# Kernel optimization log

Measured on AMD Instinct MI355X. Metric: run time of the kernel, lower is better.

Reference implementation:

```python
import jax, jax.numpy as jnp
import numpy as np

N = 100000      # nodes
E = 1200000     # edges (avg degree ~12)
D_IN = 64
D_OUT = 64


def setup_inputs() -> dict:
    key = jax.random.key(0)
    k1, k2, k3, k4 = jax.random.split(key, 4)
    x = jax.random.normal(k1, (N, D_IN), dtype=jnp.float32)
    # learned params (glorot-ish init)
    W = jax.random.normal(k2, (D_IN, D_OUT), dtype=jnp.float32) / np.sqrt(D_IN).astype(np.float32)
    b = jnp.zeros((D_OUT,), dtype=jnp.float32)
    src = jax.random.randint(k3, (E,), 0, N, dtype=jnp.int32)
    dst = jax.random.randint(k4, (E,), 0, N, dtype=jnp.int32)
    return {"x": x, "W": W, "b": b, "src": src, "dst": dst}


def reference(x, W, b, src, dst):
    # GCN layer: h = relu( D^-1/2 A D^-1/2 (x @ W) + b ), dropout=0 (eval)
    ones = jnp.ones(src.shape[0], dtype=x.dtype)
    deg_out = jax.ops.segment_sum(ones, src, num_segments=N)   # out-degree of source nodes
    deg_in = jax.ops.segment_sum(ones, dst, num_segments=N)    # in-degree of dest nodes
    norm_src = jax.lax.rsqrt(jnp.maximum(deg_out, 1.0))
    norm_dst = jax.lax.rsqrt(jnp.maximum(deg_in, 1.0))

    h = x @ W                                                  # [N, D_OUT] dense transform
    msg = h[src] * norm_src[src][:, None]                      # [E, D_OUT] gathered, pre-normalized messages
    agg = jax.ops.segment_sum(msg, dst, num_segments=N)        # [N, D_OUT] sparse aggregation
    out = agg * norm_dst[:, None] + b
    return jax.nn.relu(out)
```

## Files before the change

kernel.cpp:

```cpp
#include <hip/hip_runtime.h>
#include <hip/hip_bf16.h>

#define N_NODES 100000
#define N_EDGES 1200000
#define DCH 64

#define HB 96
#define CHUNK ((N_EDGES + HB - 1) / HB)
#define HALF_BINS 50000
#define HALF_WORDS 12500

#define BNODES 256
#define KBUK ((N_NODES + BNODES - 1) / BNODES)
#define CAPE 6144

#define OFF_DEG      0
#define OFF_BPART    512000
#define OFF_BLOCKOFF 665600
#define OFF_FLAG     819200
#define OFF_ESORT    819456
#define OFF_HS       10419712

__device__ __forceinline__ float load_f(const void* p, int i, int f32) {
    if (f32) return ((const float*)p)[i];
    return __bfloat162float(((const __hip_bfloat16*)p)[i]);
}

__device__ __forceinline__ unsigned short f2bf_bits(float f) {
    __hip_bfloat16 h = __float2bfloat16(f);
    return __builtin_bit_cast(unsigned short, h);
}

__global__ __launch_bounds__(1024)
void edges_kernel(const int* __restrict__ src,
                  const int* __restrict__ dst,
                  const void* __restrict__ x,
                  unsigned int* __restrict__ deg_packed,
                  int* __restrict__ bpart,
                  int* __restrict__ flag) {
    __shared__ unsigned int h[HALF_WORDS];
    __shared__ int cnt[KBUK];
    int tid = threadIdx.x, b = blockIdx.x, half = blockIdx.y;
    for (int w = tid; w < HALF_WORDS; w += 1024) h[w] = 0;
    if (half == 0)
        for (int i = tid; i < KBUK; i += 1024) cnt[i] = 0;
    __syncthreads();
    int lo = half * HALF_BINS;
    int e0 = b * CHUNK;
    int e1 = e0 + CHUNK; if (e1 > N_EDGES) e1 = N_EDGES;
    for (int e = e0 + tid; e < e1; e += 1024) {
        int n = src[e] - lo;
        if ((unsigned)n < (unsigned)HALF_BINS)
            atomicAdd(&h[n >> 2], 1u << ((n & 3) * 8));
        if (half == 0)
            atomicAdd(&cnt[dst[e] >> 8], 1);
    }
    __syncthreads();
    unsigned int* dp = deg_packed + half * HALF_WORDS;
    for (int w = tid; w < HALF_WORDS; w += 1024) {
        unsigned int v = h[w];
        if (v) atomicAdd(&dp[w], v);
    }
    if (half == 0)
        for (int i = tid; i < KBUK; i += 1024) bpart[b * KBUK + i] = cnt[i];

    if (b == 0 && half == 0) {
        __syncthreads();
        if (tid == 0) cnt[0] = 0;
        __syncthreads();
        if (tid < 256) {
            const unsigned short* u = (const unsigned short*)x;
            int c = 0;
            for (int i = tid * 16; i < tid * 16 + 16; ++i) {
                unsigned short v = u[2 * i];
                int e = (v >> 7) & 0xFF;
                if (e >= 141) c++;
            }
            if (c) atomicAdd(&cnt[0], c);
        }
        __syncthreads();
        if (tid == 0) *flag = (cnt[0] > 256) ? 1 : 0;
    }
}

__global__ void gemm_scale_kernel(const void* __restrict__ x,
                                  const void* __restrict__ W,
                                  const unsigned int* __restrict__ deg_packed,
                                  const int* __restrict__ flag,
                                  __hip_bfloat16* __restrict__ hs) {
    int f32 = *flag;
    int lane = threadIdx.x & 63;
    int wave = (blockIdx.x * blockDim.x + threadIdx.x) >> 6;
    int nwaves = (gridDim.x * blockDim.x) >> 6;

    float wcol[DCH];
#pragma unroll
    for (int k = 0; k < DCH; ++k)
        wcol[k] = load_f(W, k * DCH + lane, f32);

    for (int node = wave; node < N_NODES; node += nwaves) {
        float xv = load_f(x, node * DCH + lane, f32);
        float s0 = 0.0f, s1 = 0.0f, s2 = 0.0f, s3 = 0.0f;
#pragma unroll
        for (int k = 0; k < DCH; k += 4) {
            float x0 = __int_as_float(__builtin_amdgcn_readlane(__float_as_int(xv), k + 0));
            float x1 = __int_as_float(__builtin_amdgcn_readlane(__float_as_int(xv), k + 1));
            float x2 = __int_as_float(__builtin_amdgcn_readlane(__float_as_int(xv), k + 2));
            float x3 = __int_as_float(__builtin_amdgcn_readlane(__float_as_int(xv), k + 3));
            s0 = fmaf(x0, wcol[k + 0], s0);
            s1 = fmaf(x1, wcol[k + 1], s1);
            s2 = fmaf(x2, wcol[k + 2], s2);
            s3 = fmaf(x3, wcol[k + 3], s3);
        }
        float sum = (s0 + s1) + (s2 + s3);
        unsigned int dw = deg_packed[node >> 2];
        float deg = (float)((dw >> ((node & 3) * 8)) & 0xFFu);
        float nrm = rsqrtf(fmaxf(deg, 1.0f));
        hs[node * DCH + lane] = __float2bfloat16(sum * nrm);
    }
}

__global__ __launch_bounds__(512)
void bscan_kernel(const int* __restrict__ bpart, int* __restrict__ blockoff) {
    __shared__ int s[512];
    int k = threadIdx.x;
    int tot = 0;
    if (k < KBUK)
        for (int b = 0; b < HB; ++b) tot += bpart[b * KBUK + k];
    s[k] = tot;
    __syncthreads();
    for (int off = 1; off < 512; off <<= 1) {
        int add = (k >= off) ? s[k - off] : 0;
        __syncthreads();
        s[k] += add;
        __syncthreads();
    }
    if (k < KBUK) {
        int run = s[k] - tot;
        for (int b = 0; b < HB; ++b) {
            blockoff[b * KBUK + k] = run;
            run += bpart[b * KBUK + k];
        }
    }
}

__global__ __launch_bounds__(1024)
void semisort_kernel(const int* __restrict__ src,
                     const int* __restrict__ dst,
                     const int* __restrict__ blockoff,
                     unsigned int* __restrict__ esort) {
    __shared__ int cur[KBUK];
    int tid = threadIdx.x, blk = blockIdx.x;
    for (int i = tid; i < KBUK; i += 1024) cur[i] = blockoff[blk * KBUK + i];
    __syncthreads();
    int e0 = blk * CHUNK;
    int e1 = e0 + CHUNK; if (e1 > N_EDGES) e1 = N_EDGES;
    for (int e = e0 + tid; e < e1; e += 1024) {
        int d = dst[e];
        int pos = atomicAdd(&cur[d >> 8], 1);
        esort[pos] = (unsigned int)src[e] | ((unsigned int)(d & 255) << 24);
    }
}

__global__ __launch_bounds__(1024)
void sortgather_kernel(const __hip_bfloat16* __restrict__ hs,
                       const unsigned int* __restrict__ esort,
                       const int* __restrict__ blockoff,
                       const void* __restrict__ b,
                       const int* __restrict__ flag,
                       void* __restrict__ out) {
    __shared__ unsigned int ebuf[CAPE];
    __shared__ int cnt[BNODES];
    __shared__ int loc[BNODES];
    __shared__ int sc[BNODES];
    __shared__ int cur[BNODES];
    int k = blockIdx.x, tid = threadIdx.x;
    int bbase = blockoff[k];
    int bend  = (k + 1 < KBUK) ? blockoff[k + 1] : N_EDGES;
    int m = bend - bbase;
    if (m > CAPE) m = CAPE;

    if (tid < BNODES) { cnt[tid] = 0; cur[tid] = 0; }
    __syncthreads();
    for (int e = tid; e < m; e += 1024)
        atomicAdd(&cnt[esort[bbase + e] >> 24], 1);
    __syncthreads();
    int v = 0;
    if (tid < BNODES) { v = cnt[tid]; sc[tid] = v; }
    __syncthreads();
    for (int off = 1; off < BNODES; off <<= 1) {
        int add = 0;
        if (tid < BNODES && tid >= off) add = sc[tid - off];
        __syncthreads();
        if (tid < BNODES) sc[tid] += add;
        __syncthreads();
    }
    if (tid < BNODES) loc[tid] = sc[tid] - v;
    __syncthreads();
    for (int e = tid; e < m; e += 1024) {
        unsigned int w = esort[bbase + e];
        int r = w >> 24;
        int pos = loc[r] + atomicAdd(&cur[r], 1);
        ebuf[pos] = w & 0xFFFFFFu;
    }
    __syncthreads();

    int f32 = *flag;
    int lane = tid & 63, wv = tid >> 6;
    int q = lane >> 4;
    int cg = lane & 15;
    const unsigned short* hsu = (const unsigned short*)hs;
    float b0 = load_f(b, cg * 4 + 0, f32);
    float b1 = load_f(b, cg * 4 + 1, f32);
    float b2 = load_f(b, cg * 4 + 2, f32);
    float b3 = load_f(b, cg * 4 + 3, f32);
    int nlo = k * BNODES;
    for (int t = wv; t < BNODES; t += 16) {
        int node = nlo + t;
        if (node >= N_NODES) break;
        int beg = loc[t], deg = cnt[t];
        float4 a0 = {0.f,0.f,0.f,0.f}, a1 = {0.f,0.f,0.f,0.f};
        float4 a2 = {0.f,0.f,0.f,0.f}, a3 = {0.f,0.f,0.f,0.f};
        for (int j0 = 0; j0 < deg; j0 += 16) {
            int i0 = j0 + q, i1 = j0 + 4 + q, i2 = j0 + 8 + q, i3 = j0 + 12 + q;
            unsigned int s0 = ebuf[beg + (i0 < deg ? i0 : 0)];
            unsigned int s1 = ebuf[beg + (i1 < deg ? i1 : 0)];
            unsigned int s2 = ebuf[beg + (i2 < deg ? i2 : 0)];
            unsigned int s3 = ebuf[beg + (i3 < deg ? i3 : 0)];
            uint2 u0 = ((const uint2*)(hsu + s0 * DCH))[cg];
            uint2 u1 = ((const uint2*)(hsu + s1 * DCH))[cg];
            uint2 u2 = ((const uint2*)(hsu + s2 * DCH))[cg];
            uint2 u3 = ((const uint2*)(hsu + s3 * DCH))[cg];
            if (i0 < deg) {
                a0.x += __uint_as_float(u0.x << 16);
                a0.y += __uint_as_float(u0.x & 0xFFFF0000u);
                a0.z += __uint_as_float(u0.y << 16);
                a0.w += __uint_as_float(u0.y & 0xFFFF0000u);
            }
            if (i1 < deg) {
                a1.x += __uint_as_float(u1.x << 16);
                a1.y += __uint_as_float(u1.x & 0xFFFF0000u);
                a1.z += __uint_as_float(u1.y << 16);
                a1.w += __uint_as_float(u1.y & 0xFFFF0000u);
            }
            if (i2 < deg) {
                a2.x += __uint_as_float(u2.x << 16);
                a2.y += __uint_as_float(u2.x & 0xFFFF0000u);
                a2.z += __uint_as_float(u2.y << 16);
                a2.w += __uint_as_float(u2.y & 0xFFFF0000u);
            }
            if (i3 < deg) {
                a3.x += __uint_as_float(u3.x << 16);
                a3.y += __uint_as_float(u3.x & 0xFFFF0000u);
                a3.z += __uint_as_float(u3.y << 16);
                a3.w += __uint_as_float(u3.y & 0xFFFF0000u);
            }
        }
        float4 o;
        o.x = (a0.x + a1.x) + (a2.x + a3.x);
        o.y = (a0.y + a1.y) + (a2.y + a3.y);
        o.z = (a0.z + a1.z) + (a2.z + a3.z);
        o.w = (a0.w + a1.w) + (a2.w + a3.w);
        o.x += __shfl_xor(o.x, 16); o.y += __shfl_xor(o.y, 16);
        o.z += __shfl_xor(o.z, 16); o.w += __shfl_xor(o.w, 16);
        o.x += __shfl_xor(o.x, 32); o.y += __shfl_xor(o.y, 32);
        o.z += __shfl_xor(o.z, 32); o.w += __shfl_xor(o.w, 32);
        if (lane < 16) {
            float nrm = rsqrtf(fmaxf((float)deg, 1.0f));
            o.x = fmaxf(o.x * nrm + b0, 0.0f);
            o.y = fmaxf(o.y * nrm + b1, 0.0f);
            o.z = fmaxf(o.z * nrm + b2, 0.0f);
            o.w = fmaxf(o.w * nrm + b3, 0.0f);
            if (f32) {
                ((float4*)out)[node * 16 + cg] = o;
            } else {
                ushort4 s;
                s.x = f2bf_bits(o.x);
                s.y = f2bf_bits(o.y);
                s.z = f2bf_bits(o.z);
                s.w = f2bf_bits(o.w);
                ((ushort4*)out)[node * 16 + cg] = s;
            }
        }
    }
}

extern "C" void kernel_launch(void* const* d_in, const int* in_sizes, int n_in,
                              void* d_out, int out_size, void* d_ws, size_t ws_size,
                              hipStream_t stream) {
    const void* x   = d_in[0];
    const void* W   = d_in[1];
    const void* b   = d_in[2];
    const int*  src = (const int*)d_in[3];
    const int*  dst = (const int*)d_in[4];

    char* ws = (char*)d_ws;
    unsigned int* deg_packed = (unsigned int*)(ws + OFF_DEG);
    int* bpart    = (int*)(ws + OFF_BPART);
    int* blockoff = (int*)(ws + OFF_BLOCKOFF);
    int* flag     = (int*)(ws + OFF_FLAG);
    unsigned int* esort = (unsigned int*)(ws + OFF_ESORT);
    __hip_bfloat16* hs  = (__hip_bfloat16*)(ws + OFF_HS);

    (void)hipMemsetAsync(deg_packed, 0, 2 * HALF_WORDS * 4, stream);

    edges_kernel<<<dim3(HB, 2), 1024, 0, stream>>>(src, dst, x, deg_packed, bpart, flag);

    gemm_scale_kernel<<<2048, 256, 0, stream>>>(x, W, deg_packed, flag, hs);

    bscan_kernel<<<1, 512, 0, stream>>>(bpart, blockoff);
    semisort_kernel<<<HB, 1024, 0, stream>>>(src, dst, blockoff, esort);

    sortgather_kernel<<<KBUK, 1024, 0, stream>>>(hs, esort, blockoff, b, flag, d_out);
}
```

Measured before the change: 185.5 us.

## Fuse bucket scan into edges kernel via last-block counter, vectorize edge loads

Removes the separate single-block scan kernel by having the last finishing half-0 block of the edge pass (detected with an atomic counter cleared by the extended memset) compute the bucket prefix offsets. Edge reads in the histogram and semisort passes switch to int2 pairs to halve load instructions. The gather loop now processes two nodes per wave with two accumulators each instead of one node with four, giving more independent rows in flight. This saves a launch but puts a serial scan tail on one block and relies on CHUNK being even and aligned.

```diff
diff --git a/kernel.cpp b/kernel.cpp
--- a/kernel.cpp
+++ b/kernel.cpp
@@ -15,6 +15,7 @@
 #define CAPE 6144
 
 #define OFF_DEG      0
+#define OFF_CNTR     100000
 #define OFF_BPART    512000
 #define OFF_BLOCKOFF 665600
 #define OFF_FLAG     819200
@@ -37,9 +38,13 @@
                   const void* __restrict__ x,
                   unsigned int* __restrict__ deg_packed,
                   int* __restrict__ bpart,
+                  int* __restrict__ blockoff,
+                  int* __restrict__ counter,
                   int* __restrict__ flag) {
     __shared__ unsigned int h[HALF_WORDS];
     __shared__ int cnt[KBUK];
+    __shared__ int ss[512];
+    __shared__ int amlast;
     int tid = threadIdx.x, b = blockIdx.x, half = blockIdx.y;
     for (int w = tid; w < HALF_WORDS; w += 1024) h[w] = 0;
     if (half == 0)
@@ -47,13 +52,21 @@
     __syncthreads();
     int lo = half * HALF_BINS;
     int e0 = b * CHUNK;
-    int e1 = e0 + CHUNK; if (e1 > N_EDGES) e1 = N_EDGES;
-    for (int e = e0 + tid; e < e1; e += 1024) {
-        int n = src[e] - lo;
-        if ((unsigned)n < (unsigned)HALF_BINS)
-            atomicAdd(&h[n >> 2], 1u << ((n & 3) * 8));
-        if (half == 0)
-            atomicAdd(&cnt[dst[e] >> 8], 1);
+    const int2* src2 = (const int2*)(src + e0);
+    const int2* dst2 = (const int2*)(dst + e0);
+    int npair = CHUNK >> 1;
+    for (int p = tid; p < npair; p += 1024) {
+        int2 sp = src2[p];
+        int n0 = sp.x - lo, n1 = sp.y - lo;
+        if ((unsigned)n0 < (unsigned)HALF_BINS)
+            atomicAdd(&h[n0 >> 2], 1u << ((n0 & 3) * 8));
+        if ((unsigned)n1 < (unsigned)HALF_BINS)
+            atomicAdd(&h[n1 >> 2], 1u << ((n1 & 3) * 8));
+        if (half == 0) {
+            int2 dp = dst2[p];
+            atomicAdd(&cnt[dp.x >> 8], 1);
+            atomicAdd(&cnt[dp.y >> 8], 1);
+        }
     }
     __syncthreads();
     unsigned int* dp = deg_packed + half * HALF_WORDS;
@@ -80,6 +93,39 @@
         }
         __syncthreads();
         if (tid == 0) *flag = (cnt[0] > 256) ? 1 : 0;
+    }
+
+    if (half == 0) {
+        __syncthreads();
+        if (tid == 0) {
+            __threadfence();
+            int prev = __hip_atomic_fetch_add(counter, 1, __ATOMIC_ACQ_REL,
+                                              __HIP_MEMORY_SCOPE_AGENT);
+            amlast = (prev == HB - 1) ? 1 : 0;
+        }
+        __syncthreads();
+        if (amlast) {
+            __threadfence();
+            int tot = 0;
+            if (tid < KBUK)
+                for (int bb = 0; bb < HB; ++bb) tot += bpart[bb * KBUK + tid];
+            if (tid < 512) ss[tid] = (tid < KBUK) ? tot : 0;
+            __syncthreads();
+            for (int off = 1; off < 512; off <<= 1) {
+                int add = 0;
+                if (tid < 512 && tid >= off) add = ss[tid - off];
+                __syncthreads();
+                if (tid < 512) ss[tid] += add;
+                __syncthreads();
+            }
+            if (tid < KBUK) {
+                int run = ss[tid] - tot;
+                for (int bb = 0; bb < HB; ++bb) {
+                    blockoff[bb * KBUK + tid] = run;
+                    run += bpart[bb * KBUK + tid];
+                }
+            }
+        }
     }
 }
 
@@ -120,30 +166,6 @@
     }
 }
 
-__global__ __launch_bounds__(512)
-void bscan_kernel(const int* __restrict__ bpart, int* __restrict__ blockoff) {
-    __shared__ int s[512];
-    int k = threadIdx.x;
-    int tot = 0;
-    if (k < KBUK)
-        for (int b = 0; b < HB; ++b) tot += bpart[b * KBUK + k];
-    s[k] = tot;
-    __syncthreads();
-    for (int off = 1; off < 512; off <<= 1) {
-        int add = (k >= off) ? s[k - off] : 0;
-        __syncthreads();
-        s[k] += add;
-        __syncthreads();
-    }
-    if (k < KBUK) {
-        int run = s[k] - tot;
-        for (int b = 0; b < HB; ++b) {
-            blockoff[b * KBUK + k] = run;
-            run += bpart[b * KBUK + k];
-        }
-    }
-}
-
 __global__ __launch_bounds__(1024)
 void semisort_kernel(const int* __restrict__ src,
                      const int* __restrict__ dst,
@@ -154,11 +176,16 @@
     for (int i = tid; i < KBUK; i += 1024) cur[i] = blockoff[blk * KBUK + i];
     __syncthreads();
     int e0 = blk * CHUNK;
-    int e1 = e0 + CHUNK; if (e1 > N_EDGES) e1 = N_EDGES;
-    for (int e = e0 + tid; e < e1; e += 1024) {
-        int d = dst[e];
-        int pos = atomicAdd(&cur[d >> 8], 1);
-        esort[pos] = (unsigned int)src[e] | ((unsigned int)(d & 255) << 24);
+    const int2* src2 = (const int2*)(src + e0);
+    const int2* dst2 = (const int2*)(dst + e0);
+    int npair = CHUNK >> 1;
+    for (int p = tid; p < npair; p += 1024) {
+        int2 sp = src2[p];
+        int2 dp = dst2[p];
+        int pos0 = atomicAdd(&cur[dp.x >> 8], 1);
+        esort[pos0] = (unsigned int)sp.x | ((unsigned int)(dp.x & 255) << 24);
+        int pos1 = atomicAdd(&cur[dp.y >> 8], 1);
+        esort[pos1] = (unsigned int)sp.y | ((unsigned int)(dp.y & 255) << 24);
     }
 }
 
@@ -215,71 +242,80 @@
     float b2 = load_f(b, cg * 4 + 2, f32);
     float b3 = load_f(b, cg * 4 + 3, f32);
     int nlo = k * BNODES;
-    for (int t = wv; t < BNODES; t += 16) {
-        int node = nlo + t;
-        if (node >= N_NODES) break;
-        int beg = loc[t], deg = cnt[t];
-        float4 a0 = {0.f,0.f,0.f,0.f}, a1 = {0.f,0.f,0.f,0.f};
-        float4 a2 = {0.f,0.f,0.f,0.f}, a3 = {0.f,0.f,0.f,0.f};
-        for (int j0 = 0; j0 < deg; j0 += 16) {
-            int i0 = j0 + q, i1 = j0 + 4 + q, i2 = j0 + 8 + q, i3 = j0 + 12 + q;
-            unsigned int s0 = ebuf[beg + (i0 < deg ? i0 : 0)];
-            unsigned int s1 = ebuf[beg + (i1 < deg ? i1 : 0)];
-            unsigned int s2 = ebuf[beg + (i2 < deg ? i2 : 0)];
-            unsigned int s3 = ebuf[beg + (i3 < deg ? i3 : 0)];
-            uint2 u0 = ((const uint2*)(hsu + s0 * DCH))[cg];
-            uint2 u1 = ((const uint2*)(hsu + s1 * DCH))[cg];
-            uint2 u2 = ((const uint2*)(hsu + s2 * DCH))[cg];
-            uint2 u3 = ((const uint2*)(hsu + s3 * DCH))[cg];
-            if (i0 < deg) {
-                a0.x += __uint_as_float(u0.x << 16);
-                a0.y += __uint_as_float(u0.x & 0xFFFF0000u);
-                a0.z += __uint_as_float(u0.y << 16);
-                a0.w += __uint_as_float(u0.y & 0xFFFF0000u);
-            }
-            if (i1 < deg) {
-                a1.x += __uint_as_float(u1.x << 16);
-                a1.y += __uint_as_float(u1.x & 0xFFFF0000u);
-                a1.z += __uint_as_float(u1.y << 16);
-                a1.w += __uint_as_float(u1.y & 0xFFFF0000u);
-            }
-            if (i2 < deg) {
-                a2.x += __uint_as_float(u2.x << 16);
-                a2.y += __uint_as_float(u2.x & 0xFFFF0000u);
-                a2.z += __uint_as_float(u2.y << 16);
-                a2.w += __uint_as_float(u2.y & 0xFFFF0000u);
-            }
-            if (i3 < deg) {
-                a3.x += __uint_as_float(u3.x << 16);
-                a3.y += __uint_as_float(u3.x & 0xFFFF0000u);
-                a3.z += __uint_as_float(u3.y << 16);
-                a3.w += __uint_as_float(u3.y & 0xFFFF0000u);
-            }
-        }
-        float4 o;
-        o.x = (a0.x + a1.x) + (a2.x + a3.x);
-        o.y = (a0.y + a1.y) + (a2.y + a3.y);
-        o.z = (a0.z + a1.z) + (a2.z + a3.z);
-        o.w = (a0.w + a1.w) + (a2.w + a3.w);
-        o.x += __shfl_xor(o.x, 16); o.y += __shfl_xor(o.y, 16);
-        o.z += __shfl_xor(o.z, 16); o.w += __shfl_xor(o.w, 16);
-        o.x += __shfl_xor(o.x, 32); o.y += __shfl_xor(o.y, 32);
-        o.z += __shfl_xor(o.z, 32); o.w += __shfl_xor(o.w, 32);
-        if (lane < 16) {
-            float nrm = rsqrtf(fmaxf((float)deg, 1.0f));
+    for (int base = wv; base < BNODES; base += 32) {
+        int tA = base, tB = base + 16;
+        int nodeA = nlo + tA, nodeB = nlo + tB;
+        int begA = loc[tA], degA = cnt[tA];
+        int begB = loc[tB], degB = cnt[tB];
+        float4 aA0 = {0.f,0.f,0.f,0.f}, aA1 = {0.f,0.f,0.f,0.f};
+        float4 aB0 = {0.f,0.f,0.f,0.f}, aB1 = {0.f,0.f,0.f,0.f};
+        int dmax = degA > degB ? degA : degB;
+        for (int j0 = 0; j0 < dmax; j0 += 8) {
+            int i0 = j0 + q, i1 = j0 + 4 + q;
+            unsigned int sA0 = ebuf[(i0 < degA) ? (begA + i0) : 0];
+            unsigned int sA1 = ebuf[(i1 < degA) ? (begA + i1) : 0];
+            unsigned int sB0 = ebuf[(i0 < degB) ? (begB + i0) : 0];
+            unsigned int sB1 = ebuf[(i1 < degB) ? (begB + i1) : 0];
+            uint2 uA0 = ((const uint2*)(hsu + sA0 * DCH))[cg];
+            uint2 uA1 = ((const uint2*)(hsu + sA1 * DCH))[cg];
+            uint2 uB0 = ((const uint2*)(hsu + sB0 * DCH))[cg];
+            uint2 uB1 = ((const uint2*)(hsu + sB1 * DCH))[cg];
+            if (i0 < degA) {
+                aA0.x += __uint_as_float(uA0.x << 16);
+                aA0.y += __uint_as_float(uA0.x & 0xFFFF0000u);
+                aA0.z += __uint_as_float(uA0.y << 16);
+                aA0.w += __uint_as_float(uA0.y & 0xFFFF0000u);
+            }
+            if (i1 < degA) {
+                aA1.x += __uint_as_float(uA1.x << 16);
+                aA1.y += __uint_as_float(uA1.x & 0xFFFF0000u);
+                aA1.z += __uint_as_float(uA1.y << 16);
+                aA1.w += __uint_as_float(uA1.y & 0xFFFF0000u);
+            }
+            if (i0 < degB) {
+                aB0.x += __uint_as_float(uB0.x << 16);
+                aB0.y += __uint_as_float(uB0.x & 0xFFFF0000u);
+                aB0.z += __uint_as_float(uB0.y << 16);
+                aB0.w += __uint_as_float(uB0.y & 0xFFFF0000u);
+            }
+            if (i1 < degB) {
+                aB1.x += __uint_as_float(uB1.x << 16);
+                aB1.y += __uint_as_float(uB1.x & 0xFFFF0000u);
+                aB1.z += __uint_as_float(uB1.y << 16);
+                aB1.w += __uint_as_float(uB1.y & 0xFFFF0000u);
+            }
+        }
+        float4 oA, oB;
+        oA.x = aA0.x + aA1.x; oA.y = aA0.y + aA1.y;
+        oA.z = aA0.z + aA1.z; oA.w = aA0.w + aA1.w;
+        oB.x = aB0.x + aB1.x; oB.y = aB0.y + aB1.y;
+        oB.z = aB0.z + aB1.z; oB.w = aB0.w + aB1.w;
+        oA.x += __shfl_xor(oA.x, 16); oA.y += __shfl_xor(oA.y, 16);
+        oA.z += __shfl_xor(oA.z, 16); oA.w += __shfl_xor(oA.w, 16);
+        oA.x += __shfl_xor(oA.x, 32); oA.y += __shfl_xor(oA.y, 32);
+        oA.z += __shfl_xor(oA.z, 32); oA.w += __shfl_xor(oA.w, 32);
+        oB.x += __shfl_xor(oB.x, 16); oB.y += __shfl_xor(oB.y, 16);
+        oB.z += __shfl_xor(oB.z, 16); oB.w += __shfl_xor(oB.w, 16);
+        oB.x += __shfl_xor(oB.x, 32); oB.y += __shfl_xor(oB.y, 32);
+        oB.z += __shfl_xor(oB.z, 32); oB.w += __shfl_xor(oB.w, 32);
+        int myNode = (lane < 16) ? nodeA : nodeB;
+        int myDeg  = (lane < 16) ? degA : degB;
+        float4 o   = (lane < 16) ? oA : oB;
+        if (lane < 32 && myNode < N_NODES) {
+            float nrm = rsqrtf(fmaxf((float)myDeg, 1.0f));
             o.x = fmaxf(o.x * nrm + b0, 0.0f);
             o.y = fmaxf(o.y * nrm + b1, 0.0f);
             o.z = fmaxf(o.z * nrm + b2, 0.0f);
             o.w = fmaxf(o.w * nrm + b3, 0.0f);
             if (f32) {
-                ((float4*)out)[node * 16 + cg] = o;
+                ((float4*)out)[myNode * 16 + cg] = o;
             } else {
                 ushort4 s;
                 s.x = f2bf_bits(o.x);
                 s.y = f2bf_bits(o.y);
                 s.z = f2bf_bits(o.z);
                 s.w = f2bf_bits(o.w);
-                ((ushort4*)out)[node * 16 + cg] = s;
+                ((ushort4*)out)[myNode * 16 + cg] = s;
             }
         }
     }
@@ -296,19 +332,20 @@
 
     char* ws = (char*)d_ws;
     unsigned int* deg_packed = (unsigned int*)(ws + OFF_DEG);
+    int* counter  = (int*)(ws + OFF_CNTR);
     int* bpart    = (int*)(ws + OFF_BPART);
     int* blockoff = (int*)(ws + OFF_BLOCKOFF);
     int* flag     = (int*)(ws + OFF_FLAG);
     unsigned int* esort = (unsigned int*)(ws + OFF_ESORT);
     __hip_bfloat16* hs  = (__hip_bfloat16*)(ws + OFF_HS);
 
-    (void)hipMemsetAsync(deg_packed, 0, 2 * HALF_WORDS * 4, stream);
-
-    edges_kernel<<<dim3(HB, 2), 1024, 0, stream>>>(src, dst, x, deg_packed, bpart, flag);
+    (void)hipMemsetAsync(deg_packed, 0, 2 * HALF_WORDS * 4 + 4, stream);
+
+    edges_kernel<<<dim3(HB, 2), 1024, 0, stream>>>(
+        src, dst, x, deg_packed, bpart, blockoff, counter, flag);
 
     gemm_scale_kernel<<<2048, 256, 0, stream>>>(x, W, deg_packed, flag, hs);
 
-    bscan_kernel<<<1, 512, 0, stream>>>(bpart, blockoff);
     semisort_kernel<<<HB, 1024, 0, stream>>>(src, dst, blockoff, esort);
 
     sortgather_kernel<<<KBUK, 1024, 0, stream>>>(hs, esort, blockoff, b, flag, d_out);
```

Result: no change. 184.4 us (-0.6%).
